# Kernel tuning notes

Hardware: AMD Instinct MI355X
Metric: run time of the kernel (lower is better)

## Reference

```python
import jax, jax.numpy as jnp
import numpy as np

N = 100000
E = 1600000
DIMS = [64, 64, 64, 32]  # input -> hidden -> hidden -> num_classes
NEG_SLOPE = 0.01  # F.leaky_relu default


def setup_inputs() -> dict:
    key = jax.random.key(0)
    ks = jax.random.split(key, 8)
    inp = {
        "x": jax.random.normal(ks[0], (N, DIMS[0]), dtype=jnp.float32),
        "edge_index": jax.random.randint(ks[1], (2, E), 0, N, dtype=jnp.int64),
    }
    # GCNConv linear weights (glorot-ish scale) and biases
    for i in range(3):
        d_in, d_out = DIMS[i], DIMS[i + 1]
        scale = (2.0 / (d_in + d_out)) ** 0.5
        inp[f"W{i+1}"] = jax.random.normal(ks[2 + i], (d_in, d_out), dtype=jnp.float32) * scale
        inp[f"b{i+1}"] = jnp.zeros((d_out,), dtype=jnp.float32)
    return inp


def _gcn_conv(x, src, dst, norm, W, b):
    # x' = D^-1/2 (A+I) D^-1/2 (x W) + b
    h = x @ W                                   # [N, d_out]
    msg = h[src] * norm[:, None]                # gather + edge scaling  [E+N, d_out]
    out = jax.ops.segment_sum(msg, dst, num_segments=N)  # scatter-add
    return out + b


def reference(x, edge_index, W1, b1, W2, b2, W3, b3):
    loops = jnp.arange(N, dtype=edge_index.dtype)
    src = jnp.concatenate([edge_index[0], loops])  # add self-loops
    dst = jnp.concatenate([edge_index[1], loops])
    deg = jax.ops.segment_sum(jnp.ones_like(src, dtype=x.dtype), dst, num_segments=N)
    deg_isqrt = jax.lax.rsqrt(deg)              # deg >= 1 due to self-loops
    norm = deg_isqrt[src] * deg_isqrt[dst]      # [E+N]

    embeddings = []
    h = x
    for i, (W, b) in enumerate([(W1, b1), (W2, b2), (W3, b3)]):
        h = _gcn_conv(h, src, dst, norm, W, b)
        if i < 2:
            h = jnp.where(h >= 0, h, NEG_SLOPE * h)  # leaky_relu
        embeddings.append(h)
    return tuple(embeddings)
```

## Files before the change

kernel.cpp:

```cpp
#include <hip/hip_runtime.h>
#include <hip/hip_bf16.h>

typedef __hip_bfloat16 bf16;
typedef __attribute__((ext_vector_type(8))) short bf16x8;
typedef __attribute__((ext_vector_type(4))) short bf16x4;
typedef __attribute__((ext_vector_type(4))) float f32x4;

constexpr int BLK = 256;
constexpr int SCAN2_T = 512;
constexpr int NBLK = 400;

__device__ inline float s2f(short s) {
    union { unsigned u; float f; } z;
    z.u = ((unsigned)(unsigned short)s) << 16;
    return z.f;
}
__device__ inline short f2s(float f) {
    union { bf16 h; short s; } u;
    u.h = __float2bfloat16(f);
    return u.s;
}

__global__ void bucket_hist(const int* __restrict__ dst, int* __restrict__ blockhist,
                            int E, int EPB, int NB) {
    __shared__ int h[512];
    for (int i = threadIdx.x; i < NB; i += BLK) h[i] = 0;
    __syncthreads();
    int lo = blockIdx.x * EPB;
    int hi = min(E, lo + EPB);
    for (int t = lo + threadIdx.x; t < hi; t += BLK)
        atomicAdd(&h[dst[t] >> 8], 1);
    __syncthreads();
    for (int i = threadIdx.x; i < NB; i += BLK)
        blockhist[i * NBLK + blockIdx.x] = h[i];
}

__global__ void colscan_kernel(int* __restrict__ blockhist, int* __restrict__ btotal) {
    __shared__ int s[SCAN2_T];
    int b = blockIdx.x;
    int t = threadIdx.x;
    int v = (t < NBLK) ? blockhist[b * NBLK + t] : 0;
    s[t] = v;
    __syncthreads();
    for (int off = 1; off < SCAN2_T; off <<= 1) {
        int add = (t >= off) ? s[t - off] : 0;
        __syncthreads();
        s[t] += add;
        __syncthreads();
    }
    if (t < NBLK) blockhist[b * NBLK + t] = s[t] - v;
    if (t == SCAN2_T - 1) btotal[b] = s[SCAN2_T - 1];
}

__global__ void scan2_kernel(int* __restrict__ bsum, int nb) {
    __shared__ int s[SCAN2_T];
    int t = threadIdx.x;
    int v = (t < nb) ? bsum[t] : 0;
    s[t] = v;
    __syncthreads();
    for (int off = 1; off < SCAN2_T; off <<= 1) {
        int add = (t >= off) ? s[t - off] : 0;
        __syncthreads();
        s[t] += add;
        __syncthreads();
    }
    if (t < nb) bsum[t] = s[t] - v;
}

__global__ void bucket_scatter(const int* __restrict__ src, const int* __restrict__ dst,
                               const int* __restrict__ blockhist, const int* __restrict__ bbase,
                               int* __restrict__ ssd, int E, int EPB, int NB) {
    __shared__ int h[512];
    for (int i = threadIdx.x; i < NB; i += BLK)
        h[i] = bbase[i] + blockhist[i * NBLK + blockIdx.x];
    __syncthreads();
    int lo = blockIdx.x * EPB;
    int hi = min(E, lo + EPB);
    for (int t = lo + threadIdx.x; t < hi; t += BLK) {
        int d = dst[t];
        int pos = atomicAdd(&h[d >> 8], 1);
        ssd[pos] = (src[t] << 8) | (d & 255);
    }
}

__global__ void bucket_csr(const int* __restrict__ ssd, const int* __restrict__ bbase,
                           int* __restrict__ col, int* __restrict__ deg,
                           int* __restrict__ row_ptr, float* __restrict__ dinv,
                           int N, int E, int NB) {
    __shared__ int dloc[256];
    __shared__ int ss[256];
    __shared__ int cur[256];
    int b = blockIdx.x;
    int t = threadIdx.x;
    int lo = bbase[b];
    int hi = (b + 1 < NB) ? bbase[b + 1] : E;
    dloc[t] = 0;
    __syncthreads();
    for (int j = lo + t; j < hi; j += BLK)
        atomicAdd(&dloc[ssd[j] & 255], 1);
    __syncthreads();
    int own = dloc[t];
    ss[t] = own;
    __syncthreads();
    for (int off = 1; off < 256; off <<= 1) {
        int add = (t >= off) ? ss[t - off] : 0;
        __syncthreads();
        ss[t] += add;
        __syncthreads();
    }
    int excl = ss[t] - own;
    cur[t] = lo + excl;
    int node = (b << 8) + t;
    if (node < N) {
        deg[node] = own;
        row_ptr[node] = lo + excl;
        dinv[node] = rsqrtf((float)own + 1.0f);
    }
    __syncthreads();
    for (int j = lo + t; j < hi; j += BLK) {
        unsigned e = (unsigned)ssd[j];
        int p = atomicAdd(&cur[e & 255], 1);
        col[p] = (int)(e >> 8);
    }
}

__global__ void wconv_all(const float* __restrict__ W1, const float* __restrict__ W2,
                          const float* __restrict__ W3, bf16* __restrict__ WT1,
                          bf16* __restrict__ WT2, bf16* __restrict__ WT3) {
    int idx = blockIdx.x * blockDim.x + threadIdx.x;
    if (idx < 4096) {
        int k = idx >> 6, c = idx & 63;
        WT1[c * 64 + k] = __float2bfloat16(W1[idx]);
    } else if (idx < 8192) {
        int i = idx - 4096, k = i >> 6, c = i & 63;
        WT2[c * 64 + k] = __float2bfloat16(W2[i]);
    } else if (idx < 10240) {
        int i = idx - 8192, k = i >> 5, c = i & 31;
        WT3[c * 64 + k] = __float2bfloat16(W3[i]);
    }
}

template <int DOUT, bool AF32>
__global__ void mfma_gemm(const void* __restrict__ inv, const bf16* __restrict__ WT,
                          const float* __restrict__ dinv, bf16* __restrict__ hlin, int n) {
    constexpr int NT = DOUT / 16;
    const int lane = threadIdx.x & 63;
    const int wave = threadIdx.x >> 6;
    const int q = lane >> 4;
    const int l16 = lane & 15;
    const int row0 = blockIdx.x * 64 + wave * 16;

    int arow = row0 + l16;
    if (arow >= n) arow = n - 1;

    bf16x8 a0, a1;
    if (AF32) {
        const float* in = (const float*)inv;
        const float* p = in + (size_t)arow * 64 + q * 8;
        float4 f0 = *(const float4*)(p);
        float4 f1 = *(const float4*)(p + 4);
        float4 g0 = *(const float4*)(p + 32);
        float4 g1 = *(const float4*)(p + 36);
        bf16 t0[8] = {__float2bfloat16(f0.x), __float2bfloat16(f0.y), __float2bfloat16(f0.z), __float2bfloat16(f0.w),
                      __float2bfloat16(f1.x), __float2bfloat16(f1.y), __float2bfloat16(f1.z), __float2bfloat16(f1.w)};
        bf16 t1[8] = {__float2bfloat16(g0.x), __float2bfloat16(g0.y), __float2bfloat16(g0.z), __float2bfloat16(g0.w),
                      __float2bfloat16(g1.x), __float2bfloat16(g1.y), __float2bfloat16(g1.z), __float2bfloat16(g1.w)};
        __builtin_memcpy(&a0, t0, 16);
        __builtin_memcpy(&a1, t1, 16);
    } else {
        const bf16* in = (const bf16*)inv;
        a0 = *(const bf16x8*)(in + (size_t)arow * 64 + q * 8);
        a1 = *(const bf16x8*)(in + (size_t)arow * 64 + 32 + q * 8);
    }

    f32x4 acc[NT];
#pragma unroll
    for (int ct = 0; ct < NT; ++ct) {
        const bf16* wrow = WT + (size_t)(ct * 16 + l16) * 64 + q * 8;
        bf16x8 b0 = *(const bf16x8*)(wrow);
        bf16x8 b1 = *(const bf16x8*)(wrow + 32);
        f32x4 c = {0.f, 0.f, 0.f, 0.f};
        c = __builtin_amdgcn_mfma_f32_16x16x32_bf16(a0, b0, c, 0, 0, 0);
        c = __builtin_amdgcn_mfma_f32_16x16x32_bf16(a1, b1, c, 0, 0, 0);
        acc[ct] = c;
    }

    float dv[4];
#pragma unroll
    for (int r = 0; r < 4; ++r) {
        int rr = row0 + q * 4 + r;
        dv[r] = (rr < n) ? dinv[rr] : 0.0f;
    }
#pragma unroll
    for (int ct = 0; ct < NT; ++ct) {
#pragma unroll
        for (int r = 0; r < 4; ++r) {
            int rr = row0 + q * 4 + r;
            if (rr < n)
                hlin[(size_t)rr * DOUT + ct * 16 + l16] = __float2bfloat16(acc[ct][r] * dv[r]);
        }
    }
}

template <int DOUTN, bool LEAKY>
__global__ __launch_bounds__(256, 8)
void agg_gemm_kernel(const int* __restrict__ row_ptr, const int* __restrict__ deg,
                     const int* __restrict__ col, const bf16* __restrict__ hlin,
                     const float* __restrict__ dinv, const float* __restrict__ b,
                     float* __restrict__ out, const bf16* __restrict__ WTn,
                     bf16* __restrict__ hout, int n) {
    __shared__ short tile[16 * 72];
    const int wave = threadIdx.x >> 6;
    const int lane = threadIdx.x & 63;
    const int sub = lane >> 4;
    const int g = (lane >> 3) & 1;
    const int fl = lane & 7;
    const int base = blockIdx.x * 16;
    const int node = base + wave * 4 + sub;
    const int PAD = n;

    const bool valid = node < n;
    const int nc = valid ? node : n - 1;
    const int beg = row_ptr[nc];
    const int dg = valid ? deg[nc] : 0;
    const int end = beg + dg;

    float acc[8], acc2[8];
    {
        int c0 = (valid && g == 0) ? node : PAD;
        bf16x8 sv = *(const bf16x8*)(hlin + (size_t)c0 * 64 + (fl << 3));
#pragma unroll
        for (int k = 0; k < 8; ++k) { acc[k] = s2f(sv[k]); acc2[k] = 0.0f; }
    }

    int m = dg;
    m = max(m, __shfl_xor(m, 16));
    m = max(m, __shfl_xor(m, 32));
    const int iters = (m + 7) >> 3;

    int idx = beg + g;
    int c0 = col[idx     < end ? idx     : 0];
    int c1 = col[idx + 2 < end ? idx + 2 : 0];
    int c2 = col[idx + 4 < end ? idx + 4 : 0];
    int c3 = col[idx + 6 < end ? idx + 6 : 0];
    for (int j = 0; j < iters; ++j) {
        const int a0i = (idx     < end) ? c0 : PAD;
        const int a1i = (idx + 2 < end) ? c1 : PAD;
        const int a2i = (idx + 4 < end) ? c2 : PAD;
        const int a3i = (idx + 6 < end) ? c3 : PAD;
        idx += 8;
        c0 = col[idx     < end ? idx     : 0];
        c1 = col[idx + 2 < end ? idx + 2 : 0];
        c2 = col[idx + 4 < end ? idx + 4 : 0];
        c3 = col[idx + 6 < end ? idx + 6 : 0];
        bf16x8 v0 = *(const bf16x8*)(hlin + (size_t)a0i * 64 + (fl << 3));
        bf16x8 v1 = *(const bf16x8*)(hlin + (size_t)a1i * 64 + (fl << 3));
        bf16x8 v2 = *(const bf16x8*)(hlin + (size_t)a2i * 64 + (fl << 3));
        bf16x8 v3 = *(const bf16x8*)(hlin + (size_t)a3i * 64 + (fl << 3));
#pragma unroll
        for (int k = 0; k < 8; ++k) {
            acc[k]  += s2f(v0[k]) + s2f(v1[k]);
            acc2[k] += s2f(v2[k]) + s2f(v3[k]);
        }
    }

#pragma unroll
    for (int k = 0; k < 8; ++k) acc[k] += acc2[k];
#pragma unroll
    for (int k = 0; k < 8; ++k) acc[k] += __shfl_xor(acc[k], 8);

    const float dv = dinv[nc];
    const float4 bb0 = *(const float4*)(b + (fl << 3));
    const float4 bb1 = *(const float4*)(b + (fl << 3) + 4);
    float vals[8];
    vals[0] = acc[0] * dv + bb0.x;
    vals[1] = acc[1] * dv + bb0.y;
    vals[2] = acc[2] * dv + bb0.z;
    vals[3] = acc[3] * dv + bb0.w;
    vals[4] = acc[4] * dv + bb1.x;
    vals[5] = acc[5] * dv + bb1.y;
    vals[6] = acc[6] * dv + bb1.z;
    vals[7] = acc[7] * dv + bb1.w;
    if (LEAKY) {
#pragma unroll
        for (int k = 0; k < 8; ++k) vals[k] = (vals[k] >= 0.0f) ? vals[k] : 0.01f * vals[k];
    }
    if (g == 0) {
        bf16x8 ob;
#pragma unroll
        for (int k = 0; k < 8; ++k) ob[k] = f2s(vals[k]);
        *(bf16x8*)(tile + (wave * 4 + sub) * 72 + (fl << 3)) = ob;
        if (valid) {
            float* op = out + (size_t)node * 64 + (fl << 3);
            f32x4 o0 = {vals[0], vals[1], vals[2], vals[3]};
            f32x4 o1 = {vals[4], vals[5], vals[6], vals[7]};
            __builtin_nontemporal_store(o0, (f32x4*)op);
            __builtin_nontemporal_store(o1, (f32x4*)(op + 4));
        }
    }
    __syncthreads();

    const int q = sub;
    const int l16 = lane & 15;
    if (DOUTN == 64 || wave < 2) {
        bf16x8 a0 = *(const bf16x8*)(tile + l16 * 72 + q * 8);
        bf16x8 a1 = *(const bf16x8*)(tile + l16 * 72 + 32 + q * 8);
        const bf16* wrow = WTn + (size_t)(wave * 16 + l16) * 64 + q * 8;
        bf16x8 b0 = *(const bf16x8*)(wrow);
        bf16x8 b1 = *(const bf16x8*)(wrow + 32);
        f32x4 c = {0.f, 0.f, 0.f, 0.f};
        c = __builtin_amdgcn_mfma_f32_16x16x32_bf16(a0, b0, c, 0, 0, 0);
        c = __builtin_amdgcn_mfma_f32_16x16x32_bf16(a1, b1, c, 0, 0, 0);
#pragma unroll
        for (int r = 0; r < 4; ++r) {
            int rr = base + q * 4 + r;
            if (rr < n)
                hout[(size_t)rr * DOUTN + wave * 16 + l16] = __float2bfloat16(c[r] * dinv[rr]);
        }
    }
}

__global__ __launch_bounds__(256, 8)
void agg32_kernel(const int* __restrict__ row_ptr, const int* __restrict__ deg,
                  const int* __restrict__ col, const bf16* __restrict__ hlin,
                  const float* __restrict__ dinv, const float* __restrict__ b,
                  float* __restrict__ out, int n) {
    const int wid = (blockIdx.x * blockDim.x + threadIdx.x) >> 6;
    const int lane = threadIdx.x & 63;
    const int sub = lane >> 4;
    const int g = (lane >> 3) & 1;
    const int fl = lane & 7;
    const int node = wid * 4 + sub;
    const int PAD = 2 * n;

    const bool valid = node < n;
    const int nc = valid ? node : n - 1;
    const int beg = row_ptr[nc];
    const int dg = valid ? deg[nc] : 0;
    const int end = beg + dg;

    float acc[4], acc2[4];
    {
        int c0 = (valid && g == 0) ? node : PAD;
        bf16x4 sv = *(const bf16x4*)(hlin + (size_t)c0 * 32 + (fl << 2));
#pragma unroll
        for (int k = 0; k < 4; ++k) { acc[k] = s2f(sv[k]); acc2[k] = 0.0f; }
    }

    int m = dg;
    m = max(m, __shfl_xor(m, 16));
    m = max(m, __shfl_xor(m, 32));
    const int iters = (m + 7) >> 3;

    int idx = beg + g;
    int c0 = col[idx     < end ? idx     : 0];
    int c1 = col[idx + 2 < end ? idx + 2 : 0];
    int c2 = col[idx + 4 < end ? idx + 4 : 0];
    int c3 = col[idx + 6 < end ? idx + 6 : 0];
    for (int j = 0; j < iters; ++j) {
        const int a0 = (idx     < end) ? c0 : PAD;
        const int a1 = (idx + 2 < end) ? c1 : PAD;
        const int a2 = (idx + 4 < end) ? c2 : PAD;
        const int a3 = (idx + 6 < end) ? c3 : PAD;
        idx += 8;
        c0 = col[idx     < end ? idx     : 0];
        c1 = col[idx + 2 < end ? idx + 2 : 0];
        c2 = col[idx + 4 < end ? idx + 4 : 0];
        c3 = col[idx + 6 < end ? idx + 6 : 0];
        bf16x4 v0 = *(const bf16x4*)(hlin + (size_t)a0 * 32 + (fl << 2));
        bf16x4 v1 = *(const bf16x4*)(hlin + (size_t)a1 * 32 + (fl << 2));
        bf16x4 v2 = *(const bf16x4*)(hlin + (size_t)a2 * 32 + (fl << 2));
        bf16x4 v3 = *(const bf16x4*)(hlin + (size_t)a3 * 32 + (fl << 2));
#pragma unroll
        for (int k = 0; k < 4; ++k) {
            acc[k]  += s2f(v0[k]) + s2f(v1[k]);
            acc2[k] += s2f(v2[k]) + s2f(v3[k]);
        }
    }

#pragma unroll
    for (int k = 0; k < 4; ++k) acc[k] += acc2[k];
#pragma unroll
    for (int k = 0; k < 4; ++k) acc[k] += __shfl_xor(acc[k], 8);

    const float dv = dinv[nc];
    const float4 bb = *(const float4*)(b + (fl << 2));
    float vals[4];
    vals[0] = acc[0] * dv + bb.x;
    vals[1] = acc[1] * dv + bb.y;
    vals[2] = acc[2] * dv + bb.z;
    vals[3] = acc[3] * dv + bb.w;
    if (valid && g == 0) {
        f32x4 o = {vals[0], vals[1], vals[2], vals[3]};
        __builtin_nontemporal_store(o, (f32x4*)(out + (size_t)node * 32 + (fl << 2)));
    }
}

extern "C" void kernel_launch(void* const* d_in, const int* in_sizes, int n_in,
                              void* d_out, int out_size, void* d_ws, size_t ws_size,
                              hipStream_t stream) {
    const float* x  = (const float*)d_in[0];
    const int*   ei = (const int*)d_in[1];
    const float* W1 = (const float*)d_in[2];
    const float* b1 = (const float*)d_in[3];
    const float* W2 = (const float*)d_in[4];
    const float* b2 = (const float*)d_in[5];
    const float* W3 = (const float*)d_in[6];
    const float* b3 = (const float*)d_in[7];
    float* out = (float*)d_out;

    const int N = in_sizes[0] / 64;
    const int E = in_sizes[1] / 2;
    const int* src = ei;
    const int* dst = ei + E;

    const int NB  = (N + 255) >> 8;
    const int EPB = (E + NBLK - 1) / NBLK;

    char* w = (char*)d_ws;
    auto take = [&](size_t bytes) { char* p = w; w += (bytes + 15) & ~(size_t)15; return p; };
    int*   col       = (int*)take((size_t)E * 4);
    int*   ssd       = (int*)take((size_t)E * 4);
    bf16*  hlinA     = (bf16*)take(((size_t)N * 64 + 64) * 2);
    bf16*  hlinB     = (bf16*)take(((size_t)N * 64 + 64) * 2);
    bf16*  WT1       = (bf16*)take(64 * 64 * 2);
    bf16*  WT2       = (bf16*)take(64 * 64 * 2);
    bf16*  WT3       = (bf16*)take(32 * 64 * 2);
    int*   deg       = (int*)take((size_t)N * 4);
    int*   row_ptr   = (int*)take((size_t)N * 4);
    float* dinv      = (float*)take((size_t)N * 4);
    int*   blockhist = (int*)take((size_t)NB * NBLK * 4);
    int*   btotal    = (int*)take((size_t)SCAN2_T * 4);

    float* out0 = out;
    float* out1 = out + (size_t)N * 64;
    float* out2 = out + (size_t)N * 128;

    const int gemmBlocks = (N + 63) / 64;
    const int fusedBlocks = (N + 15) / 16;
    const int aggWaves = (N + 3) / 4;
    const int aggBlocks = (aggWaves * 64 + BLK - 1) / BLK;

    hipMemsetAsync(hlinA + (size_t)N * 64, 0, 128, stream);
    hipMemsetAsync(hlinB + (size_t)N * 64, 0, 128, stream);

    bucket_hist<<<NBLK, BLK, 0, stream>>>(dst, blockhist, E, EPB, NB);
    colscan_kernel<<<NB, SCAN2_T, 0, stream>>>(blockhist, btotal);
    scan2_kernel<<<1, SCAN2_T, 0, stream>>>(btotal, NB);
    bucket_scatter<<<NBLK, BLK, 0, stream>>>(src, dst, blockhist, btotal, ssd, E, EPB, NB);
    bucket_csr<<<NB, BLK, 0, stream>>>(ssd, btotal, col, deg, row_ptr, dinv, N, E, NB);

    wconv_all<<<40, BLK, 0, stream>>>(W1, W2, W3, WT1, WT2, WT3);

    mfma_gemm<64, true><<<gemmBlocks, BLK, 0, stream>>>(x, WT1, dinv, hlinA, N);

    agg_gemm_kernel<64, true><<<fusedBlocks, BLK, 0, stream>>>(
        row_ptr, deg, col, hlinA, dinv, b1, out0, WT2, hlinB, N);

    agg_gemm_kernel<32, true><<<fusedBlocks, BLK, 0, stream>>>(
        row_ptr, deg, col, hlinB, dinv, b2, out1, WT3, hlinA, N);

    agg32_kernel<<<aggBlocks, BLK, 0, stream>>>(
        row_ptr, deg, col, hlinA, dinv, b3, out2, N);
}
```

Measured before the change: 260.9 us.

## Fuse preprocessing kernels: fold scan, weight conversion, pad memsets and first GEMM

Removes the single-block scan2 launch by having bucket_scatter and bucket_csr each recompute the bucket-base exclusive scan in shared memory. The weight transpose/convert and the pad zeroing move into extra blocks of the histogram kernel, replacing two memsets and a separate launch. The layer-1 GEMM is fused into the CSR-building kernel, using the block's 256 nodes and their degree scales held in LDS. This cuts five launches and their serialization gaps. In exchange, the scan work is duplicated per block, and the CSR kernel runs with only NB (~391) blocks doing the GEMM, which lowers parallelism for that part.

```diff
diff --git a/kernel.cpp b/kernel.cpp
--- a/kernel.cpp
+++ b/kernel.cpp
@@ -21,8 +21,51 @@
     return u.s;
 }
 
-__global__ void bucket_hist(const int* __restrict__ dst, int* __restrict__ blockhist,
-                            int E, int EPB, int NB) {
+__device__ inline void load_exscan512(int* s, const int* __restrict__ btotal,
+                                      int NB, int t) {
+    int v0 = (t < NB) ? btotal[t] : 0;
+    int v1 = (t + 256 < NB) ? btotal[t + 256] : 0;
+    s[t] = v0; s[t + 256] = v1;
+    __syncthreads();
+    for (int off = 1; off < 256; off <<= 1) {
+        int a0 = (t >= off) ? s[t - off] : 0;
+        int a1 = (t >= off) ? s[256 + t - off] : 0;
+        __syncthreads();
+        s[t] += a0; s[256 + t] += a1;
+        __syncthreads();
+    }
+    int carry = s[255];
+    int inc0 = s[t], inc1 = s[256 + t];
+    __syncthreads();
+    s[t] = inc0 - v0;
+    s[256 + t] = inc1 + carry - v1;
+    __syncthreads();
+}
+
+__global__ void bucket_histw(const int* __restrict__ dst, int* __restrict__ blockhist,
+                             const float* __restrict__ W1, const float* __restrict__ W2,
+                             const float* __restrict__ W3, bf16* __restrict__ WT1,
+                             bf16* __restrict__ WT2, bf16* __restrict__ WT3,
+                             bf16* __restrict__ padA, bf16* __restrict__ padB,
+                             int E, int EPB, int NB) {
+    if (blockIdx.x >= NBLK) {
+        int idx = (blockIdx.x - NBLK) * BLK + threadIdx.x;
+        if (idx < 4096) {
+            int k = idx >> 6, c = idx & 63;
+            WT1[c * 64 + k] = __float2bfloat16(W1[idx]);
+        } else if (idx < 8192) {
+            int i = idx - 4096, k = i >> 6, c = i & 63;
+            WT2[c * 64 + k] = __float2bfloat16(W2[i]);
+        } else if (idx < 10240) {
+            int i = idx - 8192, k = i >> 5, c = i & 31;
+            WT3[c * 64 + k] = __float2bfloat16(W3[i]);
+        } else if (idx < 10304) {
+            padA[idx - 10240] = __float2bfloat16(0.0f);
+        } else if (idx < 10368) {
+            padB[idx - 10304] = __float2bfloat16(0.0f);
+        }
+        return;
+    }
     __shared__ int h[512];
     for (int i = threadIdx.x; i < NB; i += BLK) h[i] = 0;
     __syncthreads();
@@ -52,27 +95,14 @@
     if (t == SCAN2_T - 1) btotal[b] = s[SCAN2_T - 1];
 }
 
-__global__ void scan2_kernel(int* __restrict__ bsum, int nb) {
-    __shared__ int s[SCAN2_T];
-    int t = threadIdx.x;
-    int v = (t < nb) ? bsum[t] : 0;
-    s[t] = v;
-    __syncthreads();
-    for (int off = 1; off < SCAN2_T; off <<= 1) {
-        int add = (t >= off) ? s[t - off] : 0;
-        __syncthreads();
-        s[t] += add;
-        __syncthreads();
-    }
-    if (t < nb) bsum[t] = s[t] - v;
-}
-
 __global__ void bucket_scatter(const int* __restrict__ src, const int* __restrict__ dst,
-                               const int* __restrict__ blockhist, const int* __restrict__ bbase,
+                               const int* __restrict__ blockhist, const int* __restrict__ btotal,
                                int* __restrict__ ssd, int E, int EPB, int NB) {
+    __shared__ int s[512];
     __shared__ int h[512];
+    load_exscan512(s, btotal, NB, threadIdx.x);
     for (int i = threadIdx.x; i < NB; i += BLK)
-        h[i] = bbase[i] + blockhist[i * NBLK + blockIdx.x];
+        h[i] = s[i] + blockhist[i * NBLK + blockIdx.x];
     __syncthreads();
     int lo = blockIdx.x * EPB;
     int hi = min(E, lo + EPB);
@@ -83,17 +113,21 @@
     }
 }
 
-__global__ void bucket_csr(const int* __restrict__ ssd, const int* __restrict__ bbase,
-                           int* __restrict__ col, int* __restrict__ deg,
-                           int* __restrict__ row_ptr, float* __restrict__ dinv,
-                           int N, int E, int NB) {
+__global__ void bucket_csr_gemm(const int* __restrict__ ssd, const int* __restrict__ btotal,
+                                int* __restrict__ col, int* __restrict__ deg,
+                                int* __restrict__ row_ptr, float* __restrict__ dinv,
+                                const float* __restrict__ x, const bf16* __restrict__ WT1,
+                                bf16* __restrict__ hlinA, int N, int E, int NB) {
+    __shared__ int s[512];
     __shared__ int dloc[256];
     __shared__ int ss[256];
     __shared__ int cur[256];
+    __shared__ float dvs[256];
     int b = blockIdx.x;
     int t = threadIdx.x;
-    int lo = bbase[b];
-    int hi = (b + 1 < NB) ? bbase[b + 1] : E;
+    load_exscan512(s, btotal, NB, t);
+    int lo = s[b];
+    int hi = (b + 1 < NB) ? s[b + 1] : E;
     dloc[t] = 0;
     __syncthreads();
     for (int j = lo + t; j < hi; j += BLK)
@@ -111,10 +145,12 @@
     int excl = ss[t] - own;
     cur[t] = lo + excl;
     int node = (b << 8) + t;
+    float dvloc = rsqrtf((float)own + 1.0f);
+    dvs[t] = dvloc;
     if (node < N) {
         deg[node] = own;
         row_ptr[node] = lo + excl;
-        dinv[node] = rsqrtf((float)own + 1.0f);
+        dinv[node] = dvloc;
     }
     __syncthreads();
     for (int j = lo + t; j < hi; j += BLK) {
@@ -122,41 +158,19 @@
         int p = atomicAdd(&cur[e & 255], 1);
         col[p] = (int)(e >> 8);
     }
-}
-
-__global__ void wconv_all(const float* __restrict__ W1, const float* __restrict__ W2,
-                          const float* __restrict__ W3, bf16* __restrict__ WT1,
-                          bf16* __restrict__ WT2, bf16* __restrict__ WT3) {
-    int idx = blockIdx.x * blockDim.x + threadIdx.x;
-    if (idx < 4096) {
-        int k = idx >> 6, c = idx & 63;
-        WT1[c * 64 + k] = __float2bfloat16(W1[idx]);
-    } else if (idx < 8192) {
-        int i = idx - 4096, k = i >> 6, c = i & 63;
-        WT2[c * 64 + k] = __float2bfloat16(W2[i]);
-    } else if (idx < 10240) {
-        int i = idx - 8192, k = i >> 5, c = i & 31;
-        WT3[c * 64 + k] = __float2bfloat16(W3[i]);
-    }
-}
-
-template <int DOUT, bool AF32>
-__global__ void mfma_gemm(const void* __restrict__ inv, const bf16* __restrict__ WT,
-                          const float* __restrict__ dinv, bf16* __restrict__ hlin, int n) {
-    constexpr int NT = DOUT / 16;
-    const int lane = threadIdx.x & 63;
-    const int wave = threadIdx.x >> 6;
+    __syncthreads();
+
+    const int wave = t >> 6;
+    const int lane = t & 63;
     const int q = lane >> 4;
     const int l16 = lane & 15;
-    const int row0 = blockIdx.x * 64 + wave * 16;
-
-    int arow = row0 + l16;
-    if (arow >= n) arow = n - 1;
-
-    bf16x8 a0, a1;
-    if (AF32) {
-        const float* in = (const float*)inv;
-        const float* p = in + (size_t)arow * 64 + q * 8;
+#pragma unroll
+    for (int mt0 = 0; mt0 < 4; ++mt0) {
+        const int mt = wave * 4 + mt0;
+        const int rowbase = (b << 8) + mt * 16;
+        int arow = rowbase + l16;
+        if (arow >= N) arow = N - 1;
+        const float* p = x + (size_t)arow * 64 + q * 8;
         float4 f0 = *(const float4*)(p);
         float4 f1 = *(const float4*)(p + 4);
         float4 g0 = *(const float4*)(p + 32);
@@ -165,39 +179,24 @@
                       __float2bfloat16(f1.x), __float2bfloat16(f1.y), __float2bfloat16(f1.z), __float2bfloat16(f1.w)};
         bf16 t1[8] = {__float2bfloat16(g0.x), __float2bfloat16(g0.y), __float2bfloat16(g0.z), __float2bfloat16(g0.w),
                       __float2bfloat16(g1.x), __float2bfloat16(g1.y), __float2bfloat16(g1.z), __float2bfloat16(g1.w)};
+        bf16x8 a0, a1;
         __builtin_memcpy(&a0, t0, 16);
         __builtin_memcpy(&a1, t1, 16);
-    } else {
-        const bf16* in = (const bf16*)inv;
-        a0 = *(const bf16x8*)(in + (size_t)arow * 64 + q * 8);
-        a1 = *(const bf16x8*)(in + (size_t)arow * 64 + 32 + q * 8);
-    }
-
-    f32x4 acc[NT];
-#pragma unroll
-    for (int ct = 0; ct < NT; ++ct) {
-        const bf16* wrow = WT + (size_t)(ct * 16 + l16) * 64 + q * 8;
-        bf16x8 b0 = *(const bf16x8*)(wrow);
-        bf16x8 b1 = *(const bf16x8*)(wrow + 32);
-        f32x4 c = {0.f, 0.f, 0.f, 0.f};
-        c = __builtin_amdgcn_mfma_f32_16x16x32_bf16(a0, b0, c, 0, 0, 0);
-        c = __builtin_amdgcn_mfma_f32_16x16x32_bf16(a1, b1, c, 0, 0, 0);
-        acc[ct] = c;
-    }
-
-    float dv[4];
-#pragma unroll
-    for (int r = 0; r < 4; ++r) {
-        int rr = row0 + q * 4 + r;
-        dv[r] = (rr < n) ? dinv[rr] : 0.0f;
-    }
-#pragma unroll
-    for (int ct = 0; ct < NT; ++ct) {
-#pragma unroll
-        for (int r = 0; r < 4; ++r) {
-            int rr = row0 + q * 4 + r;
-            if (rr < n)
-                hlin[(size_t)rr * DOUT + ct * 16 + l16] = __float2bfloat16(acc[ct][r] * dv[r]);
+#pragma unroll
+        for (int ct = 0; ct < 4; ++ct) {
+            const bf16* wrow = WT1 + (size_t)(ct * 16 + l16) * 64 + q * 8;
+            bf16x8 b0 = *(const bf16x8*)(wrow);
+            bf16x8 b1 = *(const bf16x8*)(wrow + 32);
+            f32x4 c = {0.f, 0.f, 0.f, 0.f};
+            c = __builtin_amdgcn_mfma_f32_16x16x32_bf16(a0, b0, c, 0, 0, 0);
+            c = __builtin_amdgcn_mfma_f32_16x16x32_bf16(a1, b1, c, 0, 0, 0);
+#pragma unroll
+            for (int r = 0; r < 4; ++r) {
+                int rr = rowbase + q * 4 + r;
+                if (rr < N)
+                    hlinA[(size_t)rr * 64 + ct * 16 + l16] =
+                        __float2bfloat16(c[r] * dvs[mt * 16 + q * 4 + r]);
+            }
         }
     }
 }
@@ -436,23 +435,17 @@
     float* out1 = out + (size_t)N * 64;
     float* out2 = out + (size_t)N * 128;
 
-    const int gemmBlocks = (N + 63) / 64;
     const int fusedBlocks = (N + 15) / 16;
     const int aggWaves = (N + 3) / 4;
     const int aggBlocks = (aggWaves * 64 + BLK - 1) / BLK;
 
-    hipMemsetAsync(hlinA + (size_t)N * 64, 0, 128, stream);
-    hipMemsetAsync(hlinB + (size_t)N * 64, 0, 128, stream);
-
-    bucket_hist<<<NBLK, BLK, 0, stream>>>(dst, blockhist, E, EPB, NB);
+    bucket_histw<<<NBLK + 41, BLK, 0, stream>>>(
+        dst, blockhist, W1, W2, W3, WT1, WT2, WT3,
+        hlinA + (size_t)N * 64, hlinB + (size_t)N * 64, E, EPB, NB);
     colscan_kernel<<<NB, SCAN2_T, 0, stream>>>(blockhist, btotal);
-    scan2_kernel<<<1, SCAN2_T, 0, stream>>>(btotal, NB);
     bucket_scatter<<<NBLK, BLK, 0, stream>>>(src, dst, blockhist, btotal, ssd, E, EPB, NB);
-    bucket_csr<<<NB, BLK, 0, stream>>>(ssd, btotal, col, deg, row_ptr, dinv, N, E, NB);
-
-    wconv_all<<<40, BLK, 0, stream>>>(W1, W2, W3, WT1, WT2, WT3);
-
-    mfma_gemm<64, true><<<gemmBlocks, BLK, 0, stream>>>(x, WT1, dinv, hlinA, N);
+    bucket_csr_gemm<<<NB, BLK, 0, stream>>>(ssd, btotal, col, deg, row_ptr, dinv,
+                                            x, WT1, hlinA, N, E, NB);
 
     agg_gemm_kernel<64, true><<<fusedBlocks, BLK, 0, stream>>>(
         row_ptr, deg, col, hlinA, dinv, b1, out0, WT2, hlinB, N);
```

Measured after the change: 253.7 us. 2.7% less time.
